# Kernel tuning notes

Measured on AMD Instinct MI355X. Metric: run time of the kernel, lower is better.

Reference implementation:

```python
import jax, jax.numpy as jnp
import numpy as np

B = 128      # graphs per batch
NPG = 40     # nodes per graph (<= MAXN)
N = B * NPG  # total nodes
E = 20000    # total edges
LP = 512     # protein sequence length
NPROT = 229  # KIBA proteins
MAXN = 45    # to_dense_batch max_num_nodes


def _gcn(x, W, b, src, dst, n):
    # PyG GCNConv: symmetric-normalized adjacency with self-loops.
    xw = x @ W
    deg = jnp.zeros((n,), xw.dtype).at[dst].add(1.0) + 1.0  # +1 for self-loop
    dinv = jax.lax.rsqrt(deg)
    msg = xw[src] * (dinv[src] * dinv[dst])[:, None]
    agg = jnp.zeros_like(xw).at[dst].add(msg) + xw * (1.0 / deg)[:, None]
    return agg + b


def _to_dense_batch(x, batch, num_graphs, max_nodes):
    n = x.shape[0]
    counts = jnp.zeros((num_graphs,), jnp.int32).at[batch].add(1)
    starts = jnp.concatenate([jnp.zeros((1,), jnp.int32), jnp.cumsum(counts)[:-1].astype(jnp.int32)])
    pos = jnp.arange(n, dtype=jnp.int32) - starts[batch]
    idx = batch * max_nodes + pos
    dense = jnp.zeros((num_graphs * max_nodes, x.shape[1]), x.dtype).at[idx].set(x)
    return dense.reshape(num_graphs, max_nodes, x.shape[1])


def setup_inputs() -> dict:
    key = jax.random.key(0)
    ks = jax.random.split(key, 32)
    xav = lambda k, s: jax.random.normal(k, s, jnp.float32) * jnp.sqrt(2.0 / (s[0] + s[-1]))
    x = jax.random.normal(ks[0], (N, 78), jnp.float32)
    src = jax.random.randint(ks[1], (E,), 0, N)
    dst = (src // NPG) * NPG + jax.random.randint(ks[2], (E,), 0, NPG)  # intra-graph edges
    edge_index = jnp.stack([src, dst]).astype(jnp.int32)
    target_id = jax.random.randint(ks[3], (B,), 0, NPROT).astype(jnp.int32)
    batch = (jnp.arange(N) // NPG).astype(jnp.int32)
    proteins = jax.random.normal(ks[4], (NPROT, LP, 1280), jnp.float32) * 0.1
    return dict(
        x=x, edge_index=edge_index, target_id=target_id, batch=batch, proteins=proteins,
        gW1=xav(ks[5], (78, 128)), gb1=jnp.zeros((128,), jnp.float32),
        gW2=xav(ks[6], (128, 128)), gb2=jnp.zeros((128,), jnp.float32),
        gW3=xav(ks[7], (128, 256)), gb3=jnp.zeros((256,), jnp.float32),
        fc1_W=xav(ks[8], (256, 1024)), fc1_b=jnp.zeros((1024,), jnp.float32),
        fc2_W=xav(ks[9], (1024, 128)), fc2_b=jnp.zeros((128,), jnp.float32),
        bert1_W=xav(ks[10], (1280, 128)), bert1_b=jnp.zeros((128,), jnp.float32),
        bert2_W=xav(ks[11], (128, 128)), bert2_b=jnp.zeros((128,), jnp.float32),
        W_b=xav(ks[12], (128, 128)), W_c=xav(ks[13], (32, 128)), W_p=xav(ks[14], (32, 128)),
        w_hc=xav(ks[15], (32, 1)), w_hp=xav(ks[16], (32, 1)),
        cat1_W=xav(ks[17], (256, 1024)), cat1_b=jnp.zeros((1024,), jnp.float32),
        cat2_W=xav(ks[18], (1024, 512)), cat2_b=jnp.zeros((512,), jnp.float32),
        out_W=xav(ks[19], (512, 1)), out_b=jnp.zeros((1,), jnp.float32),
    )


def _forward(x, proteins, gW1, gb1, gW2, gb2, gW3, gb3, fc1_W, fc1_b, fc2_W, fc2_b,
             bert1_W, bert1_b, bert2_W, bert2_b, W_b, W_c, W_p, w_hc, w_hp,
             cat1_W, cat1_b, cat2_W, cat2_b, out_W, out_b,
             edge_index, target_id, batch):
    relu, tanh = jax.nn.relu, jnp.tanh
    src, dst = edge_index[0], edge_index[1]
    # --- GCN stack (dropout is identity in eval) ---
    h = relu(_gcn(x, gW1, gb1, src, dst, x.shape[0]))
    h = relu(_gcn(h, gW2, gb2, src, dst, x.shape[0]))
    h = relu(_gcn(h, gW3, gb3, src, dst, x.shape[0]))  # [N, 256]
    hd = _to_dense_batch(h, batch, B, MAXN)            # [B, 45, 256]
    hd = relu(hd @ fc1_W + fc1_b)
    hd = relu(hd @ fc2_W + fc2_b)                      # [B, 45, 128]
    xc = jnp.transpose(hd, (0, 2, 1))                  # [B, 128, 45]
    # --- protein branch ---
    t = proteins[target_id]                            # [B, LP, 1280]
    t = relu(t @ bert1_W + bert1_b)
    t = relu(t @ bert2_W + bert2_b)                    # [B, LP, 128]
    # --- parallel co-attention ---
    C = tanh(jnp.einsum('blk,km,bms->bls', t, W_b, xc))       # [B, LP, 45]
    Wcx = jnp.einsum('km,bms->bks', W_c, xc)                  # [B, 32, 45]
    Wpt = jnp.einsum('km,blm->bkl', W_p, t)                   # [B, 32, LP]
    H_c = tanh(Wcx + jnp.einsum('bkl,bls->bks', Wpt, C))      # [B, 32, 45]
    H_p = tanh(Wpt + jnp.einsum('bks,bls->bkl', Wcx, C))      # [B, 32, LP]
    a_c = jax.nn.softmax(jnp.einsum('k,bks->bs', w_hc[:, 0], H_c), axis=-1)  # [B, 45]
    a_p = jax.nn.softmax(jnp.einsum('k,bkl->bl', w_hp[:, 0], H_p), axis=-1)  # [B, LP]
    c = jnp.einsum('bs,bms->bm', a_c, xc)                     # [B, 128]
    p = jnp.einsum('bl,blm->bm', a_p, t)                      # [B, 128]
    cp = jnp.concatenate([c, p], axis=1)                      # [B, 256]
    cp = relu(cp @ cat1_W + cat1_b)
    cp = relu(cp @ cat2_W + cat2_b)
    return cp @ out_W + out_b                                 # [B, 1]


def reference(x, edge_index, target_id, batch, proteins, gW1, gb1, gW2, gb2, gW3, gb3,
              fc1_W, fc1_b, fc2_W, fc2_b, bert1_W, bert1_b, bert2_W, bert2_b,
              W_b, W_c, W_p, w_hc, w_hp, cat1_W, cat1_b, cat2_W, cat2_b, out_W, out_b):
    return _forward(x, proteins, gW1, gb1, gW2, gb2, gW3, gb3, fc1_W, fc1_b, fc2_W, fc2_b,
                    bert1_W, bert1_b, bert2_W, bert2_b, W_b, W_c, W_p, w_hc, w_hp,
                    cat1_W, cat1_b, cat2_W, cat2_b, out_W, out_b,
                    edge_index, target_id, batch)
```

## Files before the change

kernel.cpp:

```cpp
#include <hip/hip_runtime.h>
#include <hip/hip_bf16.h>

typedef __hip_bfloat16 bf16;
typedef __bf16 bf16x8 __attribute__((ext_vector_type(8)));
typedef float f32x4 __attribute__((ext_vector_type(4)));

#define NB   128
#define NPGX 40
#define NNODE 5120
#define NE   20000
#define LPX  512
#define MAXNX 45

__device__ __forceinline__ void stv(float* p, float v) { *p = v; }
__device__ __forceinline__ void stv(bf16* p, float v) { *p = __float2bfloat16(v); }
__device__ __forceinline__ ushort f2bf(float f) {
    uint x = __float_as_uint(f);
    return (ushort)((x + 0x7fffu + ((x >> 16) & 1u)) >> 16);
}
__device__ __forceinline__ float bf2f(ushort u) { return __uint_as_float(((uint)u) << 16); }

template <typename TA, typename TO, int ACT, bool GATHER>
__global__ __launch_bounds__(256) void gemm_mfma(
    const TA* __restrict__ A, const ushort* __restrict__ BT, const float* __restrict__ bias,
    TO* __restrict__ C, int M, int N, int K, const int* __restrict__ tgt)
{
    __shared__ __align__(16) ushort sA[128][40];
    __shared__ __align__(16) ushort sB[128][40];
    const int t = threadIdx.x;
    const int lane = t & 63;
    const int wave = t >> 6;
    const int wr = wave >> 1, wc = wave & 1;
    const int m0 = blockIdx.x * 128;
    const int n0 = blockIdx.y * 128;
    const int fr = lane & 15;
    const int kh = lane >> 4;

    f32x4 acc[4][4] = {};

    for (int k0 = 0; k0 < K; k0 += 32) {
        if constexpr (sizeof(TA) == 2) {
            const ushort* Ap = (const ushort*)A;
#pragma unroll
            for (int i = 0; i < 2; i++) {
                int linear = i * 2048 + t * 8;
                int row = linear >> 5, k = linear & 31;
                long gr = m0 + row;
                uint4 v = *(const uint4*)(Ap + gr * (long)K + k0 + k);
                *(uint4*)&sA[row][k] = v;
            }
        } else {
            const float* Ap = (const float*)A;
#pragma unroll
            for (int i = 0; i < 4; i++) {
                int linear = i * 1024 + t * 4;
                int row = linear >> 5, k = linear & 31;
                long gr = m0 + row;
                if (GATHER) { int bb = (int)(gr >> 9); gr = (long)tgt[bb] * LPX + (gr & 511); }
                float4 v = *(const float4*)(Ap + gr * (long)K + k0 + k);
                ushort4 h;
                h.x = f2bf(v.x); h.y = f2bf(v.y); h.z = f2bf(v.z); h.w = f2bf(v.w);
                *(ushort4*)&sA[row][k] = h;
            }
        }
#pragma unroll
        for (int i = 0; i < 2; i++) {
            int linear = i * 2048 + t * 8;
            int row = linear >> 5, k = linear & 31;
            uint4 v = *(const uint4*)(BT + (long)(n0 + row) * K + k0 + k);
            *(uint4*)&sB[row][k] = v;
        }
        __syncthreads();

        bf16x8 a[4], b[4];
#pragma unroll
        for (int mf = 0; mf < 4; mf++)
            a[mf] = *(const bf16x8*)&sA[wr * 64 + mf * 16 + fr][kh * 8];
#pragma unroll
        for (int nf = 0; nf < 4; nf++)
            b[nf] = *(const bf16x8*)&sB[wc * 64 + nf * 16 + fr][kh * 8];
#pragma unroll
        for (int mf = 0; mf < 4; mf++)
#pragma unroll
            for (int nf = 0; nf < 4; nf++)
                acc[mf][nf] = __builtin_amdgcn_mfma_f32_16x16x32_bf16(a[mf], b[nf], acc[mf][nf], 0, 0, 0);
        __syncthreads();
    }

#pragma unroll
    for (int mf = 0; mf < 4; mf++) {
#pragma unroll
        for (int nf = 0; nf < 4; nf++) {
            int coln = n0 + wc * 64 + nf * 16 + fr;
            float bv = bias ? bias[coln] : 0.f;
#pragma unroll
            for (int r = 0; r < 4; r++) {
                int row = m0 + wr * 64 + mf * 16 + kh * 4 + r;
                float v = acc[mf][nf][r] + bv;
                if (ACT == 1) v = fmaxf(v, 0.f);
                else if (ACT == 2) v = tanhf(v);
                stv(&C[(long)row * N + coln], v);
            }
        }
    }
}

__global__ __launch_bounds__(256) void k_transp_all(
    const float* __restrict__ s0, const float* __restrict__ s1, const float* __restrict__ s2,
    const float* __restrict__ s3, const float* __restrict__ s4,
    ushort* __restrict__ d0, ushort* __restrict__ d1, ushort* __restrict__ d2,
    ushort* __restrict__ d3, ushort* __restrict__ d4)
{
    __shared__ float s[32][33];
    int bid = blockIdx.x;
    const float* in; ushort* out; int K, N, b;
    if (bid < 256)      { in = s0; out = d0; K = 256;  N = 1024; b = bid; }
    else if (bid < 384) { in = s1; out = d1; K = 1024; N = 128;  b = bid - 256; }
    else if (bid < 544) { in = s2; out = d2; K = 1280; N = 128;  b = bid - 384; }
    else if (bid < 560) { in = s3; out = d3; K = 128;  N = 128;  b = bid - 544; }
    else                { in = s4; out = d4; K = 128;  N = 128;  b = bid - 560; }
    int ktiles = K / 32;
    int kt = (b % ktiles) * 32, nt = (b / ktiles) * 32;
    int t = threadIdx.x;
    int tn = t & 31, tk = t >> 5;
#pragma unroll
    for (int i = 0; i < 4; i++)
        s[tk + i * 8][tn] = in[(long)(kt + tk + i * 8) * N + nt + tn];
    __syncthreads();
#pragma unroll
    for (int i = 0; i < 4; i++)
        out[(long)(nt + tk + i * 8) * K + kt + tn] = f2bf(s[tn][tk + i * 8]);
}

__global__ void k_count(const int* __restrict__ dst, int* __restrict__ cnt, int E) {
    int e = blockIdx.x * 256 + threadIdx.x;
    if (e < E) atomicAdd(&cnt[dst[e]], 1);
}

__global__ void k_scan(const int* __restrict__ cnt, int* __restrict__ row_start,
                       float* __restrict__ dinv, float* __restrict__ deginv, int n) {
    __shared__ int sd[1024];
    __shared__ int scarry;
    int t = threadIdx.x;
    if (t == 0) scarry = 0;
    __syncthreads();
    for (int base = 0; base < n; base += 1024) {
        int i = base + t;
        int v = (i < n) ? cnt[i] : 0;
        sd[t] = v;
        __syncthreads();
        for (int off = 1; off < 1024; off <<= 1) {
            int tmp = (t >= off) ? sd[t - off] : 0;
            __syncthreads();
            sd[t] += tmp;
            __syncthreads();
        }
        int carry = scarry;
        if (i < n) {
            row_start[i] = carry + sd[t] - v;
            float deg = (float)(v + 1);
            dinv[i] = rsqrtf(deg);
            deginv[i] = 1.f / deg;
        }
        __syncthreads();
        if (t == 1023) scarry = carry + sd[1023];
        __syncthreads();
    }
    if (t == 0) row_start[n] = scarry;
}

__global__ void k_fill(const int* __restrict__ src, const int* __restrict__ dst,
                       const int* __restrict__ row_start, int* __restrict__ cursor,
                       int* __restrict__ col, float* __restrict__ val,
                       const float* __restrict__ dinv, int E) {
    int e = blockIdx.x * 256 + threadIdx.x;
    if (e >= E) return;
    int d = dst[e], s = src[e];
    int p = atomicAdd(&cursor[d], 1);
    int idx = row_start[d] + p;
    col[idx] = s;
    val[idx] = dinv[s] * dinv[d];
}

__device__ __forceinline__ void gcn_gemm(const float (*hin)[132], float (*hout)[260],
                                         float (*sW)[260], const float* __restrict__ Wg,
                                         int K, int N, int NQ, int t) {
    f32x4 acc[10] = {};
    for (int k0 = 0; k0 < K; k0 += 32) {
        int kmax = min(32, K - k0);
        __syncthreads();
        for (int o = t; o < kmax * N; o += 256) sW[o / N][o % N] = Wg[(k0 + o / N) * N + o % N];
        __syncthreads();
        for (int kk = 0; kk < kmax; kk++) {
#pragma unroll 10
            for (int j = 0; j < NQ; j++) {
                int q = t + j * 256;
                int i = q / (N / 4), f = (q % (N / 4)) * 4;
                float h = hin[i][k0 + kk];
                f32x4 wv = *(const f32x4*)&sW[kk][f];
                acc[j][0] += h * wv[0]; acc[j][1] += h * wv[1];
                acc[j][2] += h * wv[2]; acc[j][3] += h * wv[3];
            }
        }
    }
    __syncthreads();
#pragma unroll 10
    for (int j = 0; j < NQ; j++) {
        int q = t + j * 256;
        int i = q / (N / 4), f = (q % (N / 4)) * 4;
        *(f32x4*)&hout[i][f] = acc[j];
    }
}

__device__ __forceinline__ void gcn_agg(const float (*hout)[260], float (*hin)[132],
                                        const float* __restrict__ bias,
                                        const float* __restrict__ deginv,
                                        const int* __restrict__ row_start,
                                        const int* __restrict__ col,
                                        const float* __restrict__ val,
                                        float* __restrict__ hd, int N, bool tohd, int g, int t) {
    int base = g * NPGX;
    for (int o = t; o < 40 * N; o += 256) {
        int i = o / N, f = o - i * N;
        float s = hout[i][f] * deginv[base + i];
        int e0 = row_start[base + i], e1 = row_start[base + i + 1];
        for (int e = e0; e < e1; e++) s += val[e] * hout[col[e] - base][f];
        s += bias[f];
        s = fmaxf(s, 0.f);
        if (tohd) hd[(g * MAXNX + i) * N + f] = s;
        else      hin[i][f] = s;
    }
    if (tohd) for (int o = t; o < 5 * N; o += 256) hd[(g * MAXNX + 40) * N + o] = 0.f;
}

__global__ __launch_bounds__(256) void k_gcn(
    const float* __restrict__ x,
    const float* __restrict__ W1, const float* __restrict__ b1,
    const float* __restrict__ W2, const float* __restrict__ b2,
    const float* __restrict__ W3, const float* __restrict__ b3,
    const float* __restrict__ deginv, const int* __restrict__ row_start,
    const int* __restrict__ col, const float* __restrict__ val,
    float* __restrict__ hd)
{
    int g = blockIdx.x, t = threadIdx.x;
    __shared__ float hin[40][132];
    __shared__ float hout[40][260];
    __shared__ float sW[32][260];
    for (int o = t; o < 40 * 78; o += 256) hin[o / 78][o % 78] = x[(g * NPGX + o / 78) * 78 + o % 78];
    gcn_gemm(hin, hout, sW, W1, 78, 128, 5, t);
    __syncthreads();
    gcn_agg(hout, hin, b1, deginv, row_start, col, val, nullptr, 128, false, g, t);
    __syncthreads();
    gcn_gemm(hin, hout, sW, W2, 128, 128, 5, t);
    __syncthreads();
    gcn_agg(hout, hin, b2, deginv, row_start, col, val, nullptr, 128, false, g, t);
    __syncthreads();
    gcn_gemm(hin, hout, sW, W3, 128, 256, 10, t);
    __syncthreads();
    gcn_agg(hout, nullptr, b3, deginv, row_start, col, val, hd, 256, true, g, t);
}

__global__ __launch_bounds__(512) void k_coatt(
    const ushort* __restrict__ tWb, const ushort* __restrict__ t2,
    const float* __restrict__ hd2,
    const float* __restrict__ W_c, const float* __restrict__ W_p,
    const float* __restrict__ w_hc, const float* __restrict__ w_hp,
    float* __restrict__ cp)
{
    __shared__ float  sx[48][132];
    __shared__ float  sWp[32][132];
    __shared__ float  sWcx[32][48];
    __shared__ float  sHc[32][49];
    __shared__ ushort sT[128][132];
    __shared__ float  sC[128][49];
    __shared__ float  sWpt[32][132];
    __shared__ float  sLogit[512];
    __shared__ float  sLc[48];
    __shared__ float  swh[64];
    __shared__ float  sRed[8], sRed2[8];
    __shared__ float  sPc[4][128];

    const int b = blockIdx.x, tid = threadIdx.x;

    for (int o = tid; o < 45 * 128; o += 512) sx[o >> 7][o & 127] = hd2[(b * 45 + (o >> 7)) * 128 + (o & 127)];
    for (int o = tid; o < 32 * 128; o += 512) sWp[o >> 7][o & 127] = W_p[o];
    for (int o = tid; o < 32 * 128; o += 512) sWpt[o >> 7][o & 127] = W_c[o];
    if (tid < 64) swh[tid] = (tid < 32) ? w_hc[tid] : w_hp[tid - 32];
    for (int o = tid; o < 32 * 49; o += 512) (&sHc[0][0])[o] = 0.f;
    __syncthreads();

    {
        int k = tid >> 4, si = tid & 15;
        float a0 = 0.f, a1 = 0.f, a2 = 0.f;
        for (int m = 0; m < 128; m++) {
            float w = sWpt[k][m];
            a0 += w * sx[si][m]; a1 += w * sx[si + 16][m]; a2 += w * sx[si + 32][m];
        }
        sWcx[k][si] = a0; sWcx[k][si + 16] = a1;
        if (si < 13) sWcx[k][si + 32] = a2;
    }
    __syncthreads();

    const ushort* t2b  = t2  + ((size_t)b * 512) * 128;
    const ushort* tWbb = tWb + ((size_t)b * 512) * 128;

    for (int lc = 0; lc < 4; lc++) {
        {
            const ushort* src = t2b + lc * 128 * 128;
#pragma unroll
            for (int i = 0; i < 8; i++) {
                int idx = tid + i * 512;
                int row = idx >> 5, c4 = (idx & 31) * 4;
                *(uint2*)&sT[row][c4] = *(const uint2*)(src + row * 128 + c4);
            }
        }
        __syncthreads();
        {
            int kg = tid >> 5, li = tid & 31;
            float acc[8] = {};
            for (int m = 0; m < 128; m++) {
                float w0 = sWp[2 * kg][m], w1 = sWp[2 * kg + 1][m];
#pragma unroll
                for (int u = 0; u < 4; u++) {
                    float tv = bf2f(sT[li + 32 * u][m]);
                    acc[u] += w0 * tv; acc[4 + u] += w1 * tv;
                }
            }
#pragma unroll
            for (int u = 0; u < 4; u++) {
                sWpt[2 * kg][li + 32 * u] = acc[u];
                sWpt[2 * kg + 1][li + 32 * u] = acc[4 + u];
            }
        }
        __syncthreads();
        {
            const ushort* src = tWbb + lc * 128 * 128;
#pragma unroll
            for (int i = 0; i < 8; i++) {
                int idx = tid + i * 512;
                int row = idx >> 5, c4 = (idx & 31) * 4;
                *(uint2*)&sT[row][c4] = *(const uint2*)(src + row * 128 + c4);
            }
        }
        __syncthreads();
        {
            int lg = tid >> 3, sg = tid & 7;
            float acc[12] = {};
            for (int m = 0; m < 128; m++) {
                float t0 = bf2f(sT[2 * lg][m]), t1 = bf2f(sT[2 * lg + 1][m]);
#pragma unroll
                for (int u = 0; u < 6; u++) {
                    float xv = sx[6 * sg + u][m];
                    acc[u] += t0 * xv; acc[6 + u] += t1 * xv;
                }
            }
#pragma unroll
            for (int u = 0; u < 6; u++) {
                int s = 6 * sg + u;
                if (s < 45) {
                    sC[2 * lg][s] = tanhf(acc[u]);
                    sC[2 * lg + 1][s] = tanhf(acc[6 + u]);
                }
            }
        }
        __syncthreads();
        {
            int k = tid >> 4, si = tid & 15;
            float a0 = 0.f, a1 = 0.f, a2 = 0.f;
            for (int l = 0; l < 128; l++) {
                float w = sWpt[k][l];
                a0 += w * sC[l][si]; a1 += w * sC[l][si + 16]; a2 += w * sC[l][si + 32];
            }
            sHc[k][si] += a0; sHc[k][si + 16] += a1;
            if (si < 13) sHc[k][si + 32] += a2;
        }
        float hp[8];
        {
            int kg = tid >> 5, li = tid & 31;
            float acc[8] = {};
            for (int s = 0; s < 45; s++) {
                float w0 = sWcx[2 * kg][s], w1 = sWcx[2 * kg + 1][s];
#pragma unroll
                for (int u = 0; u < 4; u++) {
                    float cv = sC[li + 32 * u][s];
                    acc[u] += w0 * cv; acc[4 + u] += w1 * cv;
                }
            }
#pragma unroll
            for (int u = 0; u < 4; u++) {
                hp[u]     = tanhf(sWpt[2 * kg][li + 32 * u] + acc[u]);
                hp[4 + u] = tanhf(sWpt[2 * kg + 1][li + 32 * u] + acc[4 + u]);
            }
        }
        __syncthreads();
        {
            int kg = tid >> 5, li = tid & 31;
#pragma unroll
            for (int u = 0; u < 4; u++) {
                sWpt[2 * kg][li + 32 * u] = hp[u];
                sWpt[2 * kg + 1][li + 32 * u] = hp[4 + u];
            }
        }
        __syncthreads();
        if (tid < 128) {
            float a = 0.f;
            for (int k = 0; k < 32; k++) a += swh[32 + k] * sWpt[k][tid];
            sLogit[lc * 128 + tid] = a;
        }
        __syncthreads();
    }

    {
        int k = tid >> 4, si = tid & 15;
        sHc[k][si] = tanhf(sWcx[k][si] + sHc[k][si]);
        sHc[k][si + 16] = tanhf(sWcx[k][si + 16] + sHc[k][si + 16]);
        if (si < 13) sHc[k][si + 32] = tanhf(sWcx[k][si + 32] + sHc[k][si + 32]);
    }
    __syncthreads();
    if (tid < 45) {
        float a = 0.f;
        for (int k = 0; k < 32; k++) a += swh[k] * sHc[k][tid];
        sLc[tid] = a;
    }
    __syncthreads();
    if (tid < 64) {
        float v = (tid < 45) ? sLc[tid] : -1e30f;
        float mx = v;
        for (int off = 32; off; off >>= 1) mx = fmaxf(mx, __shfl_xor(mx, off));
        float e = (tid < 45) ? expf(v - mx) : 0.f;
        float sm = e;
        for (int off = 32; off; off >>= 1) sm += __shfl_xor(sm, off);
        if (tid < 45) sLc[tid] = e / sm;
    }
    __syncthreads();
    if (tid < 128) {
        float c = 0.f;
        for (int s = 0; s < 45; s++) c += sLc[s] * sx[s][tid];
        cp[b * 256 + tid] = c;
    }
    {
        float v = sLogit[tid];
        float mx = v;
        for (int off = 32; off; off >>= 1) mx = fmaxf(mx, __shfl_xor(mx, off));
        if ((tid & 63) == 0) sRed[tid >> 6] = mx;
        __syncthreads();
        mx = sRed[0];
#pragma unroll
        for (int w = 1; w < 8; w++) mx = fmaxf(mx, sRed[w]);
        float e = expf(v - mx);
        float sm = e;
        for (int off = 32; off; off >>= 1) sm += __shfl_xor(sm, off);
        if ((tid & 63) == 0) sRed2[tid >> 6] = sm;
        __syncthreads();
        sm = 0.f;
#pragma unroll
        for (int w = 0; w < 8; w++) sm += sRed2[w];
        sLogit[tid] = e / sm;
    }
    __syncthreads();
    {
        int gq = tid >> 7, m = tid & 127;
        float pp = 0.f;
        for (int l = gq * 128; l < gq * 128 + 128; l++)
            pp += sLogit[l] * bf2f(t2b[l * 128 + m]);
        sPc[gq][m] = pp;
    }
    __syncthreads();
    if (tid < 128)
        cp[b * 256 + 128 + tid] = sPc[0][tid] + sPc[1][tid] + sPc[2][tid] + sPc[3][tid];
}

__global__ __launch_bounds__(256) void k_head(
    const float* __restrict__ cp, const float* __restrict__ W1, const float* __restrict__ b1,
    const float* __restrict__ W2, const float* __restrict__ b2,
    const float* __restrict__ outW, const float* __restrict__ outb, float* __restrict__ out)
{
    int b = blockIdx.x, t = threadIdx.x;
    __shared__ float sin[256];
    __shared__ float s1[1024];
    __shared__ float s2[512];
    __shared__ float r[4];
    sin[t] = cp[b * 256 + t];
    __syncthreads();
#pragma unroll
    for (int j = 0; j < 4; j++) {
        int n = t + j * 256;
        float a = b1[n];
        for (int k = 0; k < 256; k++) a += sin[k] * W1[k * 1024 + n];
        s1[n] = fmaxf(a, 0.f);
    }
    __syncthreads();
#pragma unroll
    for (int j = 0; j < 2; j++) {
        int n = t + j * 256;
        float a = b2[n];
        for (int k = 0; k < 1024; k++) a += s1[k] * W2[k * 512 + n];
        s2[n] = fmaxf(a, 0.f);
    }
    __syncthreads();
    float a = 0.f;
    for (int k = t; k < 512; k += 256) a += s2[k] * outW[k];
    for (int off = 32; off; off >>= 1) a += __shfl_xor(a, off);
    if ((t & 63) == 0) r[t >> 6] = a;
    __syncthreads();
    if (t == 0) out[b] = r[0] + r[1] + r[2] + r[3] + outb[0];
}

extern "C" void kernel_launch(void* const* d_in, const int* in_sizes, int n_in,
                              void* d_out, int out_size, void* d_ws, size_t ws_size,
                              hipStream_t stream) {
    const float* x        = (const float*)d_in[0];
    const int*   ei       = (const int*)d_in[1];
    const int*   tgt      = (const int*)d_in[2];
    const float* proteins = (const float*)d_in[4];
    const float* gW1 = (const float*)d_in[5];  const float* gb1 = (const float*)d_in[6];
    const float* gW2 = (const float*)d_in[7];  const float* gb2 = (const float*)d_in[8];
    const float* gW3 = (const float*)d_in[9];  const float* gb3 = (const float*)d_in[10];
    const float* fc1_W = (const float*)d_in[11]; const float* fc1_b = (const float*)d_in[12];
    const float* fc2_W = (const float*)d_in[13]; const float* fc2_b = (const float*)d_in[14];
    const float* bert1_W = (const float*)d_in[15]; const float* bert1_b = (const float*)d_in[16];
    const float* bert2_W = (const float*)d_in[17]; const float* bert2_b = (const float*)d_in[18];
    const float* W_b = (const float*)d_in[19];
    const float* W_c = (const float*)d_in[20];
    const float* W_p = (const float*)d_in[21];
    const float* w_hc = (const float*)d_in[22];
    const float* w_hp = (const float*)d_in[23];
    const float* cat1_W = (const float*)d_in[24]; const float* cat1_b = (const float*)d_in[25];
    const float* cat2_W = (const float*)d_in[26]; const float* cat2_b = (const float*)d_in[27];
    const float* out_W = (const float*)d_in[28]; const float* out_b = (const float*)d_in[29];

    const int* src = ei;
    const int* dst = ei + NE;

    char* w = (char*)d_ws;
    auto alloc = [&](size_t bytes) -> void* {
        void* p = (void*)w;
        w += (bytes + 255) & ~(size_t)255;
        return p;
    };
    int*   cnt       = (int*)alloc((size_t)2 * NNODE * 4);
    int*   cursor    = cnt + NNODE;
    int*   row_start = (int*)alloc((NNODE + 1) * 4);
    int*   colv      = (int*)alloc(NE * 4);
    float* valv      = (float*)alloc(NE * 4);
    float* dinv      = (float*)alloc(NNODE * 4);
    float* deginv    = (float*)alloc(NNODE * 4);
    float* hd        = (float*)alloc((size_t)5760 * 256 * 4);
    bf16*  fc1o      = (bf16*)alloc((size_t)5760 * 1024 * 2);
    float* hd2       = (float*)alloc((size_t)5760 * 128 * 4);
    bf16*  t1        = (bf16*)alloc((size_t)65536 * 128 * 2);
    bf16*  t2        = (bf16*)alloc((size_t)65536 * 128 * 2);
    float* cp        = (float*)alloc((size_t)NB * 256 * 4);
    ushort* fc1_WT   = (ushort*)alloc((size_t)1024 * 256 * 2);
    ushort* fc2_WT   = (ushort*)alloc((size_t)128 * 1024 * 2);
    ushort* bert1_WT = (ushort*)alloc((size_t)128 * 1280 * 2);
    ushort* bert2_WT = (ushort*)alloc((size_t)128 * 128 * 2);
    ushort* W_bT     = (ushort*)alloc((size_t)128 * 128 * 2);
    bf16*  tWb = t1;

    k_transp_all<<<576, 256, 0, stream>>>(fc1_W, fc2_W, bert1_W, bert2_W, W_b,
                                          fc1_WT, fc2_WT, bert1_WT, bert2_WT, W_bT);
    hipMemsetAsync(cnt, 0, (size_t)2 * NNODE * 4, stream);
    k_count<<<(NE + 255) / 256, 256, 0, stream>>>(dst, cnt, NE);
    k_scan<<<1, 1024, 0, stream>>>(cnt, row_start, dinv, deginv, NNODE);
    k_fill<<<(NE + 255) / 256, 256, 0, stream>>>(src, dst, row_start, cursor, colv, valv, dinv, NE);
    k_gcn<<<NB, 256, 0, stream>>>(x, gW1, gb1, gW2, gb2, gW3, gb3,
                                  deginv, row_start, colv, valv, hd);
    gemm_mfma<float, bf16, 1, false><<<dim3(45, 8), 256, 0, stream>>>(hd, fc1_WT, fc1_b, fc1o, 5760, 1024, 256, nullptr);
    gemm_mfma<ushort, float, 1, false><<<dim3(45, 1), 256, 0, stream>>>((const ushort*)fc1o, fc2_WT, fc2_b, hd2, 5760, 128, 1024, nullptr);
    gemm_mfma<float, bf16, 1, true><<<dim3(512, 1), 256, 0, stream>>>(proteins, bert1_WT, bert1_b, t1, 65536, 128, 1280, tgt);
    gemm_mfma<ushort, bf16, 1, false><<<dim3(512, 1), 256, 0, stream>>>((const ushort*)t1, bert2_WT, bert2_b, t2, 65536, 128, 128, nullptr);
    gemm_mfma<ushort, bf16, 0, false><<<dim3(512, 1), 256, 0, stream>>>((const ushort*)t2, W_bT, nullptr, tWb, 65536, 128, 128, nullptr);
    k_coatt<<<NB, 512, 0, stream>>>((const ushort*)tWb, (const ushort*)t2, hd2,
                                    W_c, W_p, w_hc, w_hp, cp);
    k_head<<<NB, 256, 0, stream>>>(cp, cat1_W, cat1_b, cat2_W, cat2_b, out_W, out_b, (float*)d_out);
}
```

Baseline: 1.271 ms.

## Reassociate co-attention to drop tWb GEMM and use MFMA inside coatt

Result: faster. 1.240 ms (-2.4%).

```diff
diff --git a/kernel.cpp b/kernel.cpp
--- a/kernel.cpp
+++ b/kernel.cpp
@@ -19,6 +19,9 @@
     return (ushort)((x + 0x7fffu + ((x >> 16) & 1u)) >> 16);
 }
 __device__ __forceinline__ float bf2f(ushort u) { return __uint_as_float(((uint)u) << 16); }
+__device__ __forceinline__ float dot4(f32x4 a, f32x4 b) {
+    return a[0]*b[0] + a[1]*b[1] + a[2]*b[2] + a[3]*b[3];
+}
 
 template <typename TA, typename TO, int ACT, bool GATHER>
 __global__ __launch_bounds__(256) void gemm_mfma(
@@ -107,9 +110,9 @@
 
 __global__ __launch_bounds__(256) void k_transp_all(
     const float* __restrict__ s0, const float* __restrict__ s1, const float* __restrict__ s2,
-    const float* __restrict__ s3, const float* __restrict__ s4,
+    const float* __restrict__ s3,
     ushort* __restrict__ d0, ushort* __restrict__ d1, ushort* __restrict__ d2,
-    ushort* __restrict__ d3, ushort* __restrict__ d4)
+    ushort* __restrict__ d3)
 {
     __shared__ float s[32][33];
     int bid = blockIdx.x;
@@ -117,8 +120,7 @@
     if (bid < 256)      { in = s0; out = d0; K = 256;  N = 1024; b = bid; }
     else if (bid < 384) { in = s1; out = d1; K = 1024; N = 128;  b = bid - 256; }
     else if (bid < 544) { in = s2; out = d2; K = 1280; N = 128;  b = bid - 384; }
-    else if (bid < 560) { in = s3; out = d3; K = 128;  N = 128;  b = bid - 544; }
-    else                { in = s4; out = d4; K = 128;  N = 128;  b = bid - 560; }
+    else                { in = s3; out = d3; K = 128;  N = 128;  b = bid - 544; }
     int ktiles = K / 32;
     int kt = (b % ktiles) * 32, nt = (b / ktiles) * 32;
     int t = threadIdx.x;
@@ -188,18 +190,27 @@
     f32x4 acc[10] = {};
     for (int k0 = 0; k0 < K; k0 += 32) {
         int kmax = min(32, K - k0);
-        __syncthreads();
-        for (int o = t; o < kmax * N; o += 256) sW[o / N][o % N] = Wg[(k0 + o / N) * N + o % N];
-        __syncthreads();
-        for (int kk = 0; kk < kmax; kk++) {
+        int kpad = (kmax + 3) & ~3;
+        __syncthreads();
+        for (int o = t; o < kpad * N; o += 256) {
+            int row = o / N, c = o - row * N;
+            sW[row][c] = (row < kmax) ? Wg[(k0 + row) * N + c] : 0.f;
+        }
+        __syncthreads();
+        for (int kk = 0; kk < kpad; kk += 4) {
 #pragma unroll 10
             for (int j = 0; j < NQ; j++) {
                 int q = t + j * 256;
                 int i = q / (N / 4), f = (q % (N / 4)) * 4;
-                float h = hin[i][k0 + kk];
-                f32x4 wv = *(const f32x4*)&sW[kk][f];
-                acc[j][0] += h * wv[0]; acc[j][1] += h * wv[1];
-                acc[j][2] += h * wv[2]; acc[j][3] += h * wv[3];
+                f32x4 hv = *(const f32x4*)&hin[i][k0 + kk];
+#pragma unroll
+                for (int d = 0; d < 4; d++) {
+                    f32x4 wv = *(const f32x4*)&sW[kk + d][f];
+                    acc[j][0] = fmaf(hv[d], wv[0], acc[j][0]);
+                    acc[j][1] = fmaf(hv[d], wv[1], acc[j][1]);
+                    acc[j][2] = fmaf(hv[d], wv[2], acc[j][2]);
+                    acc[j][3] = fmaf(hv[d], wv[3], acc[j][3]);
+                }
             }
         }
     }
@@ -243,10 +254,11 @@
     float* __restrict__ hd)
 {
     int g = blockIdx.x, t = threadIdx.x;
-    __shared__ float hin[40][132];
-    __shared__ float hout[40][260];
-    __shared__ float sW[32][260];
+    __shared__ __align__(16) float hin[40][132];
+    __shared__ __align__(16) float hout[40][260];
+    __shared__ __align__(16) float sW[32][260];
     for (int o = t; o < 40 * 78; o += 256) hin[o / 78][o % 78] = x[(g * NPGX + o / 78) * 78 + o % 78];
+    for (int o = t; o < 80; o += 256) hin[o >> 1][78 + (o & 1)] = 0.f;
     gcn_gemm(hin, hout, sW, W1, 78, 128, 5, t);
     __syncthreads();
     gcn_agg(hout, hin, b1, deginv, row_start, col, val, nullptr, 128, false, g, t);
@@ -261,144 +273,163 @@
 }
 
 __global__ __launch_bounds__(512) void k_coatt(
-    const ushort* __restrict__ tWb, const ushort* __restrict__ t2,
-    const float* __restrict__ hd2,
-    const float* __restrict__ W_c, const float* __restrict__ W_p,
-    const float* __restrict__ w_hc, const float* __restrict__ w_hp,
-    float* __restrict__ cp)
+    const ushort* __restrict__ t2, const float* __restrict__ hd2,
+    const float* __restrict__ W_b, const float* __restrict__ W_c,
+    const float* __restrict__ W_p, const float* __restrict__ w_hc,
+    const float* __restrict__ w_hp, float* __restrict__ cp)
 {
-    __shared__ float  sx[48][132];
-    __shared__ float  sWp[32][132];
-    __shared__ float  sWcx[32][48];
-    __shared__ float  sHc[32][49];
-    __shared__ ushort sT[128][132];
-    __shared__ float  sC[128][49];
-    __shared__ float  sWpt[32][132];
+    __shared__ __align__(16) float  sx[48][132];
+    __shared__ __align__(16) ushort sY[48][136];
+    __shared__ __align__(16) ushort sWpb[32][136];
+    __shared__ __align__(16) float  sWcx[32][48];
+    __shared__ __align__(16) float  sHc[32][48];
+    __shared__ __align__(16) ushort sT[128][136];
+    __shared__ __align__(16) float  sC[128][52];
+    __shared__ __align__(16) float  sWpt[32][132];
     __shared__ float  sLogit[512];
-    __shared__ float  sLc[48];
+    __shared__ float  sLc[64];
     __shared__ float  swh[64];
     __shared__ float  sRed[8], sRed2[8];
     __shared__ float  sPc[4][128];
 
     const int b = blockIdx.x, tid = threadIdx.x;
-
-    for (int o = tid; o < 45 * 128; o += 512) sx[o >> 7][o & 127] = hd2[(b * 45 + (o >> 7)) * 128 + (o & 127)];
-    for (int o = tid; o < 32 * 128; o += 512) sWp[o >> 7][o & 127] = W_p[o];
-    for (int o = tid; o < 32 * 128; o += 512) sWpt[o >> 7][o & 127] = W_c[o];
+    const int lane = tid & 63, wave = tid >> 6;
+    const int fr = lane & 15, kh = lane >> 4;
+
+    for (int o = tid; o < 48 * 32; o += 512) {
+        int r = o >> 5, q = (o & 31) * 4;
+        f32x4 v = {0.f, 0.f, 0.f, 0.f};
+        if (r < 45) v = *(const f32x4*)&hd2[(b * 45 + r) * 128 + q];
+        *(f32x4*)&sx[r][q] = v;
+    }
+    for (int o = tid; o < 32 * 32; o += 512) {
+        int r = o >> 5, q = (o & 31) * 4;
+        f32x4 v = *(const f32x4*)&W_p[r * 128 + q];
+        sWpb[r][q] = f2bf(v[0]); sWpb[r][q + 1] = f2bf(v[1]);
+        sWpb[r][q + 2] = f2bf(v[2]); sWpb[r][q + 3] = f2bf(v[3]);
+    }
     if (tid < 64) swh[tid] = (tid < 32) ? w_hc[tid] : w_hp[tid - 32];
-    for (int o = tid; o < 32 * 49; o += 512) (&sHc[0][0])[o] = 0.f;
+    for (int o = tid; o < 32 * 12; o += 512) {
+        int r = o / 12, q = (o - r * 12) * 4;
+        *(f32x4*)&sHc[r][q] = f32x4{0.f, 0.f, 0.f, 0.f};
+    }
     __syncthreads();
 
     {
-        int k = tid >> 4, si = tid & 15;
-        float a0 = 0.f, a1 = 0.f, a2 = 0.f;
-        for (int m = 0; m < 128; m++) {
-            float w = sWpt[k][m];
-            a0 += w * sx[si][m]; a1 += w * sx[si + 16][m]; a2 += w * sx[si + 32][m];
-        }
-        sWcx[k][si] = a0; sWcx[k][si + 16] = a1;
-        if (si < 13) sWcx[k][si + 32] = a2;
-    }
-    __syncthreads();
-
-    const ushort* t2b  = t2  + ((size_t)b * 512) * 128;
-    const ushort* tWbb = tWb + ((size_t)b * 512) * 128;
+        int kg = tid >> 3, sg = tid & 7;
+        float acc[12] = {};
+        for (int m = 0; m < 128; m += 4) {
+            f32x4 w0 = *(const f32x4*)&W_b[(2 * kg) * 128 + m];
+            f32x4 w1 = *(const f32x4*)&W_b[(2 * kg + 1) * 128 + m];
+#pragma unroll
+            for (int u = 0; u < 6; u++) {
+                f32x4 xv = *(const f32x4*)&sx[6 * sg + u][m];
+                acc[u] += dot4(w0, xv);
+                acc[6 + u] += dot4(w1, xv);
+            }
+        }
+#pragma unroll
+        for (int u = 0; u < 6; u++) {
+            int s = 6 * sg + u;
+            sY[s][2 * kg] = f2bf(acc[u]);
+            sY[s][2 * kg + 1] = f2bf(acc[6 + u]);
+        }
+    }
+    if (tid < 256) {
+        int k = tid >> 3, sg = tid & 7;
+        float acc[6] = {};
+        for (int m = 0; m < 128; m += 4) {
+            f32x4 w = *(const f32x4*)&W_c[k * 128 + m];
+#pragma unroll
+            for (int u = 0; u < 6; u++) {
+                f32x4 xv = *(const f32x4*)&sx[6 * sg + u][m];
+                acc[u] += dot4(w, xv);
+            }
+        }
+#pragma unroll
+        for (int u = 0; u < 6; u++) sWcx[k][6 * sg + u] = acc[u];
+    }
+    __syncthreads();
+
+    const ushort* t2b = t2 + ((size_t)b * 512) * 128;
 
     for (int lc = 0; lc < 4; lc++) {
         {
-            const ushort* src = t2b + lc * 128 * 128;
-#pragma unroll
-            for (int i = 0; i < 8; i++) {
+            const ushort* srcp = t2b + lc * 128 * 128;
+#pragma unroll
+            for (int i = 0; i < 4; i++) {
                 int idx = tid + i * 512;
-                int row = idx >> 5, c4 = (idx & 31) * 4;
-                *(uint2*)&sT[row][c4] = *(const uint2*)(src + row * 128 + c4);
-            }
+                int row = idx >> 4, c8 = (idx & 15) * 8;
+                *(uint4*)&sT[row][c8] = *(const uint4*)(srcp + row * 128 + c8);
+            }
+        }
+        __syncthreads();
+        {
+            f32x4 cacc[3] = {};
+            f32x4 wacc[2] = {};
+#pragma unroll
+            for (int ks = 0; ks < 4; ks++) {
+                bf16x8 af = *(const bf16x8*)&sT[wave * 16 + fr][ks * 32 + kh * 8];
+#pragma unroll
+                for (int nt = 0; nt < 3; nt++) {
+                    bf16x8 bf = *(const bf16x8*)&sY[nt * 16 + fr][ks * 32 + kh * 8];
+                    cacc[nt] = __builtin_amdgcn_mfma_f32_16x16x32_bf16(af, bf, cacc[nt], 0, 0, 0);
+                }
+#pragma unroll
+                for (int mt = 0; mt < 2; mt++) {
+                    bf16x8 aw = *(const bf16x8*)&sWpb[mt * 16 + fr][ks * 32 + kh * 8];
+                    wacc[mt] = __builtin_amdgcn_mfma_f32_16x16x32_bf16(aw, af, wacc[mt], 0, 0, 0);
+                }
+            }
+#pragma unroll
+            for (int nt = 0; nt < 3; nt++)
+#pragma unroll
+                for (int r = 0; r < 4; r++)
+                    sC[wave * 16 + kh * 4 + r][nt * 16 + fr] = tanhf(cacc[nt][r]);
+#pragma unroll
+            for (int mt = 0; mt < 2; mt++)
+#pragma unroll
+                for (int r = 0; r < 4; r++)
+                    sWpt[mt * 16 + kh * 4 + r][wave * 16 + fr] = wacc[mt][r];
+        }
+        __syncthreads();
+        float hpacc[8];
+        {
+            if (tid < 384) {
+                int k = tid / 12, sg = tid - (tid / 12) * 12;
+                f32x4 a = {0.f, 0.f, 0.f, 0.f};
+                for (int l = 0; l < 128; l++) {
+                    float wv = sWpt[k][l];
+                    f32x4 cv = *(const f32x4*)&sC[l][sg * 4];
+                    a[0] = fmaf(wv, cv[0], a[0]); a[1] = fmaf(wv, cv[1], a[1]);
+                    a[2] = fmaf(wv, cv[2], a[2]); a[3] = fmaf(wv, cv[3], a[3]);
+                }
+                f32x4 h = *(const f32x4*)&sHc[k][sg * 4];
+                h[0] += a[0]; h[1] += a[1]; h[2] += a[2]; h[3] += a[3];
+                *(f32x4*)&sHc[k][sg * 4] = h;
+            }
+            int kg = tid >> 5, li = tid & 31;
+            float acc[8] = {};
+            for (int s4 = 0; s4 < 48; s4 += 4) {
+                f32x4 w0 = *(const f32x4*)&sWcx[2 * kg][s4];
+                f32x4 w1 = *(const f32x4*)&sWcx[2 * kg + 1][s4];
+#pragma unroll
+                for (int u = 0; u < 4; u++) {
+                    f32x4 cv = *(const f32x4*)&sC[li + 32 * u][s4];
+                    acc[u] += dot4(w0, cv);
+                    acc[4 + u] += dot4(w1, cv);
+                }
+            }
+#pragma unroll
+            for (int u = 0; u < 8; u++) hpacc[u] = acc[u];
         }
         __syncthreads();
         {
             int kg = tid >> 5, li = tid & 31;
-            float acc[8] = {};
-            for (int m = 0; m < 128; m++) {
-                float w0 = sWp[2 * kg][m], w1 = sWp[2 * kg + 1][m];
-#pragma unroll
-                for (int u = 0; u < 4; u++) {
-                    float tv = bf2f(sT[li + 32 * u][m]);
-                    acc[u] += w0 * tv; acc[4 + u] += w1 * tv;
-                }
-            }
 #pragma unroll
             for (int u = 0; u < 4; u++) {
-                sWpt[2 * kg][li + 32 * u] = acc[u];
-                sWpt[2 * kg + 1][li + 32 * u] = acc[4 + u];
-            }
-        }
-        __syncthreads();
-        {
-            const ushort* src = tWbb + lc * 128 * 128;
-#pragma unroll
-            for (int i = 0; i < 8; i++) {
-                int idx = tid + i * 512;
-                int row = idx >> 5, c4 = (idx & 31) * 4;
-                *(uint2*)&sT[row][c4] = *(const uint2*)(src + row * 128 + c4);
-            }
-        }
-        __syncthreads();
-        {
-            int lg = tid >> 3, sg = tid & 7;
-            float acc[12] = {};
-            for (int m = 0; m < 128; m++) {
-                float t0 = bf2f(sT[2 * lg][m]), t1 = bf2f(sT[2 * lg + 1][m]);
-#pragma unroll
-                for (int u = 0; u < 6; u++) {
-                    float xv = sx[6 * sg + u][m];
-                    acc[u] += t0 * xv; acc[6 + u] += t1 * xv;
-                }
-            }
-#pragma unroll
-            for (int u = 0; u < 6; u++) {
-                int s = 6 * sg + u;
-                if (s < 45) {
-                    sC[2 * lg][s] = tanhf(acc[u]);
-                    sC[2 * lg + 1][s] = tanhf(acc[6 + u]);
-                }
-            }
-        }
-        __syncthreads();
-        {
-            int k = tid >> 4, si = tid & 15;
-            float a0 = 0.f, a1 = 0.f, a2 = 0.f;
-            for (int l = 0; l < 128; l++) {
-                float w = sWpt[k][l];
-                a0 += w * sC[l][si]; a1 += w * sC[l][si + 16]; a2 += w * sC[l][si + 32];
-            }
-            sHc[k][si] += a0; sHc[k][si + 16] += a1;
-            if (si < 13) sHc[k][si + 32] += a2;
-        }
-        float hp[8];
-        {
-            int kg = tid >> 5, li = tid & 31;
-            float acc[8] = {};
-            for (int s = 0; s < 45; s++) {
-                float w0 = sWcx[2 * kg][s], w1 = sWcx[2 * kg + 1][s];
-#pragma unroll
-                for (int u = 0; u < 4; u++) {
-                    float cv = sC[li + 32 * u][s];
-                    acc[u] += w0 * cv; acc[4 + u] += w1 * cv;
-                }
-            }
-#pragma unroll
-            for (int u = 0; u < 4; u++) {
-                hp[u]     = tanhf(sWpt[2 * kg][li + 32 * u] + acc[u]);
-                hp[4 + u] = tanhf(sWpt[2 * kg + 1][li + 32 * u] + acc[4 + u]);
-            }
-        }
-        __syncthreads();
-        {
-            int kg = tid >> 5, li = tid & 31;
-#pragma unroll
-            for (int u = 0; u < 4; u++) {
-                sWpt[2 * kg][li + 32 * u] = hp[u];
-                sWpt[2 * kg + 1][li + 32 * u] = hp[4 + u];
+                sWpt[2 * kg][li + 32 * u] = tanhf(sWpt[2 * kg][li + 32 * u] + hpacc[u]);
+                sWpt[2 * kg + 1][li + 32 * u] = tanhf(sWpt[2 * kg + 1][li + 32 * u] + hpacc[4 + u]);
             }
         }
         __syncthreads();
@@ -412,9 +443,11 @@
 
     {
         int k = tid >> 4, si = tid & 15;
-        sHc[k][si] = tanhf(sWcx[k][si] + sHc[k][si]);
-        sHc[k][si + 16] = tanhf(sWcx[k][si + 16] + sHc[k][si + 16]);
-        if (si < 13) sHc[k][si + 32] = tanhf(sWcx[k][si + 32] + sHc[k][si + 32]);
+        if (tid < 512) {
+            sHc[k][si] = tanhf(sWcx[k][si] + sHc[k][si]);
+            sHc[k][si + 16] = tanhf(sWcx[k][si + 16] + sHc[k][si + 16]);
+            sHc[k][si + 32] = tanhf(sWcx[k][si + 32] + sHc[k][si + 32]);
+        }
     }
     __syncthreads();
     if (tid < 45) {
@@ -555,11 +588,9 @@
     ushort* fc2_WT   = (ushort*)alloc((size_t)128 * 1024 * 2);
     ushort* bert1_WT = (ushort*)alloc((size_t)128 * 1280 * 2);
     ushort* bert2_WT = (ushort*)alloc((size_t)128 * 128 * 2);
-    ushort* W_bT     = (ushort*)alloc((size_t)128 * 128 * 2);
-    bf16*  tWb = t1;
-
-    k_transp_all<<<576, 256, 0, stream>>>(fc1_W, fc2_W, bert1_W, bert2_W, W_b,
-                                          fc1_WT, fc2_WT, bert1_WT, bert2_WT, W_bT);
+
+    k_transp_all<<<560, 256, 0, stream>>>(fc1_W, fc2_W, bert1_W, bert2_W,
+                                          fc1_WT, fc2_WT, bert1_WT, bert2_WT);
     hipMemsetAsync(cnt, 0, (size_t)2 * NNODE * 4, stream);
     k_count<<<(NE + 255) / 256, 256, 0, stream>>>(dst, cnt, NE);
     k_scan<<<1, 1024, 0, stream>>>(cnt, row_start, dinv, deginv, NNODE);
@@ -570,8 +601,6 @@
     gemm_mfma<ushort, float, 1, false><<<dim3(45, 1), 256, 0, stream>>>((const ushort*)fc1o, fc2_WT, fc2_b, hd2, 5760, 128, 1024, nullptr);
     gemm_mfma<float, bf16, 1, true><<<dim3(512, 1), 256, 0, stream>>>(proteins, bert1_WT, bert1_b, t1, 65536, 128, 1280, tgt);
     gemm_mfma<ushort, bf16, 1, false><<<dim3(512, 1), 256, 0, stream>>>((const ushort*)t1, bert2_WT, bert2_b, t2, 65536, 128, 128, nullptr);
-    gemm_mfma<ushort, bf16, 0, false><<<dim3(512, 1), 256, 0, stream>>>((const ushort*)t2, W_bT, nullptr, tWb, 65536, 128, 128, nullptr);
-    k_coatt<<<NB, 512, 0, stream>>>((const ushort*)tWb, (const ushort*)t2, hd2,
-                                    W_c, W_p, w_hc, w_hp, cp);
+    k_coatt<<<NB, 512, 0, stream>>>((const ushort*)t2, hd2, W_b, W_c, W_p, w_hc, w_hp, cp);
     k_head<<<NB, 256, 0, stream>>>(cp, cat1_W, cat1_b, cat2_W, cat2_b, out_W, out_b, (float*)d_out);
 }
```
